# Kernel tuning notes

Measured on AMD Instinct MI355X. Metric: run time of the kernel, lower is better.

## Reference

```python
import jax, jax.numpy as jnp
import numpy as np

BASE_MARGIN = 0.1
N = 8192


def setup_inputs() -> dict:
    key = jax.random.key(0)
    k1, k2, k3 = jax.random.split(key, 3)
    predictions = jax.random.normal(k1, (N,), dtype=jnp.float32)
    targets = jax.random.normal(k2, (N,), dtype=jnp.float32)
    uncertainties = jax.random.uniform(k3, (N,), dtype=jnp.float32)
    return {"predictions": predictions, "targets": targets, "uncertainties": uncertainties}


def reference(predictions, targets, uncertainties):
    n = predictions.shape[0]
    # pairwise differences, [n, n]; entry (i, j) corresponds to pair (i, j)
    tdiff = targets[:, None] - targets[None, :]
    pdiff = predictions[:, None] - predictions[None, :]
    # adaptive margin: base_margin * clamp(|t_i - t_j|, 0.1, 1.0)
    margin = BASE_MARGIN * jnp.clip(jnp.abs(tdiff), 0.1, 1.0)
    # uncertainty weight: 1 / (1 + u_i + u_j)
    weight = 1.0 / (1.0 + uncertainties[:, None] + uncertainties[None, :])
    # if t_i > t_j: hinge(p_j - p_i + margin) = hinge(-pdiff + margin)
    # if t_j > t_i: hinge(p_i - p_j + margin) = hinge(+pdiff + margin)
    sgn = jnp.sign(tdiff)
    hinge = jnp.maximum(-sgn * pdiff + margin, 0.0)
    # only upper-triangular pairs (i < j) with t_i != t_j contribute
    iu = jnp.triu(jnp.ones((n, n), dtype=bool), k=1)
    mask = iu & (tdiff != 0.0)
    loss = jnp.sum(jnp.where(mask, weight * hinge, 0.0))
    count = jnp.sum(mask)
    return loss / jnp.maximum(count, 1).astype(loss.dtype)
```

## Files before the change

kernel.cpp:

```cpp
#include <hip/hip_runtime.h>


constexpr int BLOCK = 256;
constexpr int TJ    = 256;

__global__ __launch_bounds__(BLOCK) void arl_pair_kernel(
    const float* __restrict__ pred, const float* __restrict__ targ,
    const float* __restrict__ unc, int n,
    double* __restrict__ loss_out, unsigned long long* __restrict__ cnt_out)
{
    __shared__ float sp[TJ], st[TJ], su[TJ];
    const int tid = threadIdx.x;
    const int i   = blockIdx.x * BLOCK + tid;
    const int j0  = blockIdx.y * TJ;

    {
        const int j = j0 + tid;
        const bool v = j < n;
        sp[tid] = v ? pred[j] : 0.0f;
        st[tid] = v ? targ[j] : 0.0f;
        su[tid] = v ? unc[j]  : 0.0f;
    }
    __syncthreads();

    float acc = 0.0f;
    unsigned cnt = 0;

    if (i < n) {
        const float pi  = pred[i];
        const float ti  = targ[i];
        const float ui1 = 1.0f + unc[i];
        const int jmax = (n - j0 < TJ) ? (n - j0) : TJ;
        #pragma unroll 8
        for (int jj = 0; jj < jmax; ++jj) {
            const float tj = st[jj];
            const float pj = sp[jj];
            const float uj = su[jj];
            const float tdiff = ti - tj;
            const float pdiff = pi - pj;
            const float a      = fabsf(tdiff);
            const float margin = 0.1f * fminf(fmaxf(a, 0.1f), 1.0f);
            const float spd = (tdiff < 0.0f) ? -pdiff : pdiff;
            const float h   = fmaxf(margin - spd, 0.0f);
            const float w   = __builtin_amdgcn_rcpf(ui1 + uj);
            if (tdiff != 0.0f) {
                acc += w * h;
                cnt += 1u;
            }
        }
    }

    int icnt = (int)cnt;
    for (int off = 32; off > 0; off >>= 1) {
        acc  += __shfl_down(acc, off);
        icnt += __shfl_down(icnt, off);
    }

    __shared__ float    wacc[BLOCK / 64];
    __shared__ unsigned wcnt[BLOCK / 64];
    const int lane = tid & 63;
    const int wid  = tid >> 6;
    if (lane == 0) { wacc[wid] = acc; wcnt[wid] = (unsigned)icnt; }
    __syncthreads();

    if (tid == 0) {
        float a2 = 0.0f;
        unsigned long long c2 = 0;
        #pragma unroll
        for (int w = 0; w < BLOCK / 64; ++w) { a2 += wacc[w]; c2 += wcnt[w]; }
        atomicAdd(loss_out, (double)a2);
        atomicAdd(cnt_out, c2);
    }
}

__global__ void arl_finalize(const double* __restrict__ loss,
                             const unsigned long long* __restrict__ cnt,
                             float* __restrict__ out)
{
    const unsigned long long c = *cnt;
    const double denom = (double)(c ? c : 1ull);
    out[0] = (float)(*loss / denom);
}

extern "C" void kernel_launch(void* const* d_in, const int* in_sizes, int n_in,
                              void* d_out, int out_size, void* d_ws, size_t ws_size,
                              hipStream_t stream) {
    const float* pred = (const float*)d_in[0];
    const float* targ = (const float*)d_in[1];
    const float* unc  = (const float*)d_in[2];
    const int n = in_sizes[0];

    double* loss = (double*)d_ws;
    unsigned long long* cnt = (unsigned long long*)((char*)d_ws + 8);

    hipMemsetAsync(d_ws, 0, 16, stream);

    dim3 grid((n + BLOCK - 1) / BLOCK, (n + TJ - 1) / TJ);
    arl_pair_kernel<<<grid, BLOCK, 0, stream>>>(pred, targ, unc, n, loss, cnt);
    arl_finalize<<<1, 1, 0, stream>>>(loss, cnt, (float*)d_out);
}
```

Before: 93.87 us.

## Read j-tile directly from global memory and streamline inner-loop arithmetic

Removes the shared-memory staging of the j tile and its barrier, so each iteration loads pred/targ/unc[j] straight from global memory. These addresses are uniform across the wavefront and may become scalar loads. The margin clamp becomes a single fmed3 plus an fma, and the branch is replaced by a select with fma accumulation. The count is kept in float and rounded at the end, which stays exact for at most 256 pairs per thread. The loop unroll is raised to 16.

```diff
diff --git a/kernel.cpp b/kernel.cpp
--- a/kernel.cpp
+++ b/kernel.cpp
@@ -9,67 +9,54 @@
     const float* __restrict__ unc, int n,
     double* __restrict__ loss_out, unsigned long long* __restrict__ cnt_out)
 {
-    __shared__ float sp[TJ], st[TJ], su[TJ];
     const int tid = threadIdx.x;
     const int i   = blockIdx.x * BLOCK + tid;
     const int j0  = blockIdx.y * TJ;
 
-    {
-        const int j = j0 + tid;
-        const bool v = j < n;
-        sp[tid] = v ? pred[j] : 0.0f;
-        st[tid] = v ? targ[j] : 0.0f;
-        su[tid] = v ? unc[j]  : 0.0f;
-    }
-    __syncthreads();
-
-    float acc = 0.0f;
-    unsigned cnt = 0;
+    float acc  = 0.0f;
+    float cntf = 0.0f;
 
     if (i < n) {
         const float pi  = pred[i];
         const float ti  = targ[i];
         const float ui1 = 1.0f + unc[i];
         const int jmax = (n - j0 < TJ) ? (n - j0) : TJ;
-        #pragma unroll 8
+        #pragma unroll 16
         for (int jj = 0; jj < jmax; ++jj) {
-            const float tj = st[jj];
-            const float pj = sp[jj];
-            const float uj = su[jj];
+            const float tj = targ[j0 + jj];
+            const float pj = pred[j0 + jj];
+            const float uj = unc[j0 + jj];
             const float tdiff = ti - tj;
             const float pdiff = pi - pj;
-            const float a      = fabsf(tdiff);
-            const float margin = 0.1f * fminf(fmaxf(a, 0.1f), 1.0f);
+            const float m3  = __builtin_amdgcn_fmed3f(fabsf(tdiff), 0.1f, 1.0f);
             const float spd = (tdiff < 0.0f) ? -pdiff : pdiff;
-            const float h   = fmaxf(margin - spd, 0.0f);
+            const float h   = fmaxf(fmaf(m3, 0.1f, -spd), 0.0f);
             const float w   = __builtin_amdgcn_rcpf(ui1 + uj);
-            if (tdiff != 0.0f) {
-                acc += w * h;
-                cnt += 1u;
-            }
+            const bool  nz  = (tdiff != 0.0f);
+            const float hm  = nz ? h : 0.0f;
+            acc  = fmaf(w, hm, acc);
+            cntf += nz ? 1.0f : 0.0f;
         }
     }
 
-    int icnt = (int)cnt;
     for (int off = 32; off > 0; off >>= 1) {
         acc  += __shfl_down(acc, off);
-        icnt += __shfl_down(icnt, off);
+        cntf += __shfl_down(cntf, off);
     }
 
-    __shared__ float    wacc[BLOCK / 64];
-    __shared__ unsigned wcnt[BLOCK / 64];
+    __shared__ float wacc[BLOCK / 64];
+    __shared__ float wcnt[BLOCK / 64];
     const int lane = tid & 63;
     const int wid  = tid >> 6;
-    if (lane == 0) { wacc[wid] = acc; wcnt[wid] = (unsigned)icnt; }
+    if (lane == 0) { wacc[wid] = acc; wcnt[wid] = cntf; }
     __syncthreads();
 
     if (tid == 0) {
-        float a2 = 0.0f;
-        unsigned long long c2 = 0;
+        float a2 = 0.0f, c2 = 0.0f;
         #pragma unroll
         for (int w = 0; w < BLOCK / 64; ++w) { a2 += wacc[w]; c2 += wcnt[w]; }
         atomicAdd(loss_out, (double)a2);
-        atomicAdd(cnt_out, c2);
+        atomicAdd(cnt_out, (unsigned long long)(c2 + 0.5f));
     }
 }
 
```

New measurement: 94.43 us. No clear change (+0.6%).
